# Optimization experiments

Measured on AMD Instinct MI355X. Metric: run time of the kernel, lower is better.

Reference implementation:

```python
import jax, jax.numpy as jnp
import numpy as np

N_NODES = 50000
N_EDGES = 600000
D = 128  # in_channels == out_channels
LN_EPS = 1e-5


def _mlp(h, W1, b1, W2, b2, ln_g, ln_b):
    # anemoi MLP: Linear -> SiLU -> Linear -> LayerNorm
    h = jax.nn.silu(h @ W1 + b1)
    h = h @ W2 + b2
    mu = jnp.mean(h, axis=-1, keepdims=True)
    var = jnp.var(h, axis=-1, keepdims=True)
    return (h - mu) * jax.lax.rsqrt(var + LN_EPS) * ln_g + ln_b


def setup_inputs() -> dict:
    key = jax.random.key(0)
    ks = jax.random.split(key, 12)
    s = lambda fan_in: 1.0 / np.sqrt(fan_in)
    inp = {
        "x": jax.random.normal(ks[0], (N_NODES, D), dtype=jnp.float32),
        "edge_attr": jax.random.normal(ks[1], (N_EDGES, D), dtype=jnp.float32),
        "edge_index": jax.random.randint(ks[2], (2, N_EDGES), 0, N_NODES, dtype=jnp.int32),
        # conv edge-MLP params: in = 3*D (x_dst, x_src, edge_attr)
        "eW1": jax.random.uniform(ks[3], (3 * D, D), jnp.float32, -s(3 * D), s(3 * D)),
        "eb1": jnp.zeros((D,), jnp.float32),
        "eW2": jax.random.uniform(ks[4], (D, D), jnp.float32, -s(D), s(D)),
        "eb2": jnp.zeros((D,), jnp.float32),
        "eln_g": jnp.ones((D,), jnp.float32),
        "eln_b": jnp.zeros((D,), jnp.float32),
        # node MLP params: in = 2*D (x, aggregated messages)
        "nW1": jax.random.uniform(ks[5], (2 * D, D), jnp.float32, -s(2 * D), s(2 * D)),
        "nb1": jnp.zeros((D,), jnp.float32),
        "nW2": jax.random.uniform(ks[6], (D, D), jnp.float32, -s(D), s(D)),
        "nb2": jnp.zeros((D,), jnp.float32),
        "nln_g": jnp.ones((D,), jnp.float32),
        "nln_b": jnp.zeros((D,), jnp.float32),
    }
    return inp


def reference(x, edge_attr, edge_index,
              eW1, eb1, eW2, eb2, eln_g, eln_b,
              nW1, nb1, nW2, nb2, nln_g, nln_b):
    src = edge_index[0]  # j
    dst = edge_index[1]  # i
    # GraphConv.message: edge MLP over cat([x_i, x_j, edge_attr])
    edge_in = jnp.concatenate([x[dst], x[src], edge_attr], axis=1)  # [E, 3D]
    edges_new = _mlp(edge_in, eW1, eb1, eW2, eb2, eln_g, eln_b)      # [E, D]
    # aggregate: scatter-add to destination nodes (chunking sums to the same result)
    out = jax.ops.segment_sum(edges_new, dst, num_segments=x.shape[0])  # [N, D]
    # node update: concat + MLP + residual
    nodes_new = _mlp(jnp.concatenate([x, out], axis=1), nW1, nb1, nW2, nb2, nln_g, nln_b) + x
    return nodes_new, edges_new
```

## Files before the change

kernel.cpp:

```cpp
#include <hip/hip_runtime.h>

#define D       128
#define NNODES  50000
#define NEDGES  600000
#define TE      64
#define BLK     256
#define LN_EPS  1e-5f

typedef float  fx4    __attribute__((ext_vector_type(4)));
typedef float  f32x4  __attribute__((ext_vector_type(4)));
typedef __bf16 bf16x4 __attribute__((ext_vector_type(4)));
typedef __bf16 bf16x8 __attribute__((ext_vector_type(8)));

#define EW1F_OFF 0
#define EW2F_OFF (128 * 384)
#define NW1F_OFF (EW2F_OFF + 128 * 128)
#define NW2F_OFF (NW1F_OFF + 128 * 256)
#define WS_ELEMS (NW2F_OFF + 128 * 128)

__device__ __forceinline__ float silu_f(float z) {
    return z * (1.0f / (1.0f + __expf(-z)));
}

__global__ __launch_bounds__(256) void prep_weights(
    const float* __restrict__ eW1, const float* __restrict__ eW2,
    const float* __restrict__ nW1, const float* __restrict__ nW2,
    __bf16* __restrict__ ws)
{
    int idx = blockIdx.x * 256 + threadIdx.x;
    if (idx >= WS_ELEMS) return;
    const float* src;
    int local;
    if (idx < EW2F_OFF)      { src = eW1; local = idx; }
    else if (idx < NW1F_OFF) { src = eW2; local = idx - EW2F_OFF; }
    else if (idx < NW2F_OFF) { src = nW1; local = idx - NW1F_OFF; }
    else                     { src = nW2; local = idx - NW2F_OFF; }
    const int f   = local >> 9;
    const int rem = local & 511;
    const int l   = rem >> 3;
    const int j   = rem & 7;
    const int ks  = f >> 3;
    const int nf  = f & 7;
    const int n   = (nf << 4) + (l & 15);
    const int k   = (ks << 5) + ((l >> 4) << 3) + j;
    ws[idx] = (__bf16)src[(size_t)k * D + n];
}

__global__ __launch_bounds__(BLK) void edge_kernel(
    const float* __restrict__ x,
    const float* __restrict__ edge_attr,
    const int*   __restrict__ edge_index,
    const __bf16* __restrict__ W1f,
    const float* __restrict__ b1,
    const __bf16* __restrict__ W2f,
    const float* __restrict__ b2,
    const float* __restrict__ lng, const float* __restrict__ lnb,
    float* __restrict__ edges_out,
    float* __restrict__ agg)
{
    __shared__ __bf16 in_t[TE][392];
    __shared__ int    src_s[TE], dst_s[TE];

    const int tid = threadIdx.x;
    const int e0g = blockIdx.x * TE;

    if (tid < TE) {
        src_s[tid] = edge_index[e0g + tid];
        dst_s[tid] = edge_index[NEDGES + e0g + tid];
    }
    __syncthreads();

    #pragma unroll
    for (int it = 0; it < 8; ++it) {
        const int idx = tid + it * BLK;
        const int e   = idx >> 5;
        const int c4  = (idx & 31) << 2;
        fx4 v = *(const fx4*)&x[(size_t)dst_s[e] * D + c4];
        bf16x4 h;
        #pragma unroll
        for (int j = 0; j < 4; ++j) h[j] = (__bf16)v[j];
        *(bf16x4*)&in_t[e][c4] = h;
    }
    #pragma unroll
    for (int it = 0; it < 8; ++it) {
        const int idx = tid + it * BLK;
        const int e   = idx >> 5;
        const int c4  = (idx & 31) << 2;
        fx4 v = *(const fx4*)&x[(size_t)src_s[e] * D + c4];
        bf16x4 h;
        #pragma unroll
        for (int j = 0; j < 4; ++j) h[j] = (__bf16)v[j];
        *(bf16x4*)&in_t[e][128 + c4] = h;
    }
    #pragma unroll
    for (int it = 0; it < 8; ++it) {
        const int idx = tid + it * BLK;
        const int e   = idx >> 5;
        const int c4  = (idx & 31) << 2;
        fx4 v = *(const fx4*)&edge_attr[(size_t)(e0g + e) * D + c4];
        bf16x4 h;
        #pragma unroll
        for (int j = 0; j < 4; ++j) h[j] = (__bf16)v[j];
        *(bf16x4*)&in_t[e][256 + c4] = h;
    }
    __syncthreads();

    const int lane  = tid & 63;
    const int wid   = tid >> 6;
    const int wrow0 = wid << 4;
    const int c16   = lane & 15;
    const int kq    = lane >> 4;
    const int ks8   = kq << 3;
    const int lo8   = lane << 3;

    f32x4 acc[8];
    #pragma unroll
    for (int nf = 0; nf < 8; ++nf) acc[nf] = (f32x4){0.f, 0.f, 0.f, 0.f};

    #pragma unroll
    for (int ks = 0; ks < 12; ++ks) {
        bf16x8 a = *(const bf16x8*)&in_t[wrow0 + c16][(ks << 5) + ks8];
        const __bf16* wp = W1f + ((size_t)(ks << 3) << 9) + lo8;
        #pragma unroll
        for (int nf = 0; nf < 8; ++nf) {
            bf16x8 b = *(const bf16x8*)(wp + (nf << 9));
            acc[nf] = __builtin_amdgcn_mfma_f32_16x16x32_bf16(a, b, acc[nf], 0, 0, 0);
        }
    }

    #pragma unroll
    for (int nf = 0; nf < 8; ++nf) {
        const float bb = b1[nf * 16 + c16];
        #pragma unroll
        for (int r = 0; r < 4; ++r) {
            float h = silu_f(acc[nf][r] + bb);
            in_t[wrow0 + kq * 4 + r][nf * 16 + c16] = (__bf16)h;
        }
    }

    f32x4 acc2[8];
    #pragma unroll
    for (int nf = 0; nf < 8; ++nf) acc2[nf] = (f32x4){0.f, 0.f, 0.f, 0.f};

    #pragma unroll
    for (int ks = 0; ks < 4; ++ks) {
        bf16x8 a = *(const bf16x8*)&in_t[wrow0 + c16][(ks << 5) + ks8];
        const __bf16* wp = W2f + ((size_t)(ks << 3) << 9) + lo8;
        #pragma unroll
        for (int nf = 0; nf < 8; ++nf) {
            bf16x8 b = *(const bf16x8*)(wp + (nf << 9));
            acc2[nf] = __builtin_amdgcn_mfma_f32_16x16x32_bf16(a, b, acc2[nf], 0, 0, 0);
        }
    }

    float b2v[8], gv[8], bvv[8];
    #pragma unroll
    for (int nf = 0; nf < 8; ++nf) {
        b2v[nf] = b2[nf * 16 + c16];
        gv[nf]  = lng[nf * 16 + c16];
        bvv[nf] = lnb[nf * 16 + c16];
    }

    float z[8][4];
    float s[4] = {0.f, 0.f, 0.f, 0.f}, q[4] = {0.f, 0.f, 0.f, 0.f};
    #pragma unroll
    for (int nf = 0; nf < 8; ++nf)
        #pragma unroll
        for (int r = 0; r < 4; ++r) {
            float zz = acc2[nf][r] + b2v[nf];
            z[nf][r] = zz;
            s[r] += zz;
            q[r] += zz * zz;
        }
    #pragma unroll
    for (int m = 1; m <= 8; m <<= 1)
        #pragma unroll
        for (int r = 0; r < 4; ++r) {
            s[r] += __shfl_xor(s[r], m, 64);
            q[r] += __shfl_xor(q[r], m, 64);
        }
    float mu[4], rstd[4];
    #pragma unroll
    for (int r = 0; r < 4; ++r) {
        mu[r] = s[r] * (1.0f / 128.0f);
        float var = q[r] * (1.0f / 128.0f) - mu[r] * mu[r];
        rstd[r] = rsqrtf(var + LN_EPS);
    }

    #pragma unroll
    for (int r = 0; r < 4; ++r) {
        const int row = wrow0 + kq * 4 + r;
        const size_t erow = (size_t)(e0g + row) * D;
        float* ap = agg + (size_t)dst_s[row] * D;
        #pragma unroll
        for (int nf = 0; nf < 8; ++nf) {
            const int col = nf * 16 + c16;
            float o = (z[nf][r] - mu[r]) * rstd[r] * gv[nf] + bvv[nf];
            edges_out[erow + col] = o;
            atomicAdd(ap + col, o);
        }
    }
}

__global__ __launch_bounds__(BLK) void node_kernel(
    const float* __restrict__ x,
    const float* __restrict__ agg,
    const __bf16* __restrict__ W1f,
    const float* __restrict__ b1,
    const __bf16* __restrict__ W2f,
    const float* __restrict__ b2,
    const float* __restrict__ lng, const float* __restrict__ lnb,
    float* __restrict__ nodes_out)
{
    __shared__ __bf16 in_t[TE][264];

    const int tid = threadIdx.x;
    const int r0g = blockIdx.x * TE;

    #pragma unroll
    for (int it = 0; it < 8; ++it) {
        const int idx = tid + it * BLK;
        const int e   = idx >> 5;
        const int c4  = (idx & 31) << 2;
        const int row = r0g + e;
        fx4 v = {0.f, 0.f, 0.f, 0.f};
        if (row < NNODES) v = *(const fx4*)&x[(size_t)row * D + c4];
        bf16x4 h;
        #pragma unroll
        for (int j = 0; j < 4; ++j) h[j] = (__bf16)v[j];
        *(bf16x4*)&in_t[e][c4] = h;
    }
    #pragma unroll
    for (int it = 0; it < 8; ++it) {
        const int idx = tid + it * BLK;
        const int e   = idx >> 5;
        const int c4  = (idx & 31) << 2;
        const int row = r0g + e;
        fx4 v = {0.f, 0.f, 0.f, 0.f};
        if (row < NNODES) v = *(const fx4*)&agg[(size_t)row * D + c4];
        bf16x4 h;
        #pragma unroll
        for (int j = 0; j < 4; ++j) h[j] = (__bf16)v[j];
        *(bf16x4*)&in_t[e][128 + c4] = h;
    }
    __syncthreads();

    const int lane  = tid & 63;
    const int wid   = tid >> 6;
    const int wrow0 = wid << 4;
    const int c16   = lane & 15;
    const int kq    = lane >> 4;
    const int ks8   = kq << 3;
    const int lo8   = lane << 3;

    f32x4 acc[8];
    #pragma unroll
    for (int nf = 0; nf < 8; ++nf) acc[nf] = (f32x4){0.f, 0.f, 0.f, 0.f};

    #pragma unroll
    for (int ks = 0; ks < 8; ++ks) {
        bf16x8 a = *(const bf16x8*)&in_t[wrow0 + c16][(ks << 5) + ks8];
        const __bf16* wp = W1f + ((size_t)(ks << 3) << 9) + lo8;
        #pragma unroll
        for (int nf = 0; nf < 8; ++nf) {
            bf16x8 b = *(const bf16x8*)(wp + (nf << 9));
            acc[nf] = __builtin_amdgcn_mfma_f32_16x16x32_bf16(a, b, acc[nf], 0, 0, 0);
        }
    }

    #pragma unroll
    for (int nf = 0; nf < 8; ++nf) {
        const float bb = b1[nf * 16 + c16];
        #pragma unroll
        for (int r = 0; r < 4; ++r) {
            float h = silu_f(acc[nf][r] + bb);
            in_t[wrow0 + kq * 4 + r][nf * 16 + c16] = (__bf16)h;
        }
    }

    f32x4 acc2[8];
    #pragma unroll
    for (int nf = 0; nf < 8; ++nf) acc2[nf] = (f32x4){0.f, 0.f, 0.f, 0.f};

    #pragma unroll
    for (int ks = 0; ks < 4; ++ks) {
        bf16x8 a = *(const bf16x8*)&in_t[wrow0 + c16][(ks << 5) + ks8];
        const __bf16* wp = W2f + ((size_t)(ks << 3) << 9) + lo8;
        #pragma unroll
        for (int nf = 0; nf < 8; ++nf) {
            bf16x8 b = *(const bf16x8*)(wp + (nf << 9));
            acc2[nf] = __builtin_amdgcn_mfma_f32_16x16x32_bf16(a, b, acc2[nf], 0, 0, 0);
        }
    }

    float b2v[8], gv[8], bvv[8];
    #pragma unroll
    for (int nf = 0; nf < 8; ++nf) {
        b2v[nf] = b2[nf * 16 + c16];
        gv[nf]  = lng[nf * 16 + c16];
        bvv[nf] = lnb[nf * 16 + c16];
    }

    float z[8][4];
    float s[4] = {0.f, 0.f, 0.f, 0.f}, q[4] = {0.f, 0.f, 0.f, 0.f};
    #pragma unroll
    for (int nf = 0; nf < 8; ++nf)
        #pragma unroll
        for (int r = 0; r < 4; ++r) {
            float zz = acc2[nf][r] + b2v[nf];
            z[nf][r] = zz;
            s[r] += zz;
            q[r] += zz * zz;
        }
    #pragma unroll
    for (int m = 1; m <= 8; m <<= 1)
        #pragma unroll
        for (int r = 0; r < 4; ++r) {
            s[r] += __shfl_xor(s[r], m, 64);
            q[r] += __shfl_xor(q[r], m, 64);
        }
    float mu[4], rstd[4];
    #pragma unroll
    for (int r = 0; r < 4; ++r) {
        mu[r] = s[r] * (1.0f / 128.0f);
        float var = q[r] * (1.0f / 128.0f) - mu[r] * mu[r];
        rstd[r] = rsqrtf(var + LN_EPS);
    }

    #pragma unroll
    for (int r = 0; r < 4; ++r) {
        const int row = r0g + wrow0 + kq * 4 + r;
        if (row >= NNODES) continue;
        const size_t orow = (size_t)row * D;
        #pragma unroll
        for (int nf = 0; nf < 8; ++nf) {
            const int col = nf * 16 + c16;
            float o = (z[nf][r] - mu[r]) * rstd[r] * gv[nf] + bvv[nf] + x[orow + col];
            nodes_out[orow + col] = o;
        }
    }
}

extern "C" void kernel_launch(void* const* d_in, const int* in_sizes, int n_in,
                              void* d_out, int out_size, void* d_ws, size_t ws_size,
                              hipStream_t stream) {
    (void)in_sizes; (void)n_in; (void)ws_size; (void)out_size;

    const float* x         = (const float*)d_in[0];
    const float* edge_attr = (const float*)d_in[1];
    const int*   edge_idx  = (const int*)  d_in[2];
    const float* eW1 = (const float*)d_in[3];
    const float* eb1 = (const float*)d_in[4];
    const float* eW2 = (const float*)d_in[5];
    const float* eb2 = (const float*)d_in[6];
    const float* elg = (const float*)d_in[7];
    const float* elb = (const float*)d_in[8];
    const float* nW1 = (const float*)d_in[9];
    const float* nb1 = (const float*)d_in[10];
    const float* nW2 = (const float*)d_in[11];
    const float* nb2 = (const float*)d_in[12];
    const float* nlg = (const float*)d_in[13];
    const float* nlb = (const float*)d_in[14];

    float* out       = (float*)d_out;
    float* nodes_out = out;
    float* edges_out = out + (size_t)NNODES * D;

    __bf16* ws = (__bf16*)d_ws;

    prep_weights<<<(WS_ELEMS + 255) / 256, 256, 0, stream>>>(eW1, eW2, nW1, nW2, ws);

    hipMemsetAsync(nodes_out, 0, (size_t)NNODES * D * sizeof(float), stream);

    edge_kernel<<<NEDGES / TE, BLK, 0, stream>>>(
        x, edge_attr, edge_idx,
        ws + EW1F_OFF, eb1, ws + EW2F_OFF, eb2, elg, elb,
        edges_out, nodes_out);

    node_kernel<<<(NNODES + TE - 1) / TE, BLK, 0, stream>>>(
        x, nodes_out,
        ws + NW1F_OFF, nb1, ws + NW2F_OFF, nb2, nlg, nlb,
        nodes_out);
}
```

Before: 441.3 us.

## Double edge tile per block and stream K-segments through smaller shared buffer

The edge kernel now handles 128 edges per block, with each wave computing two 16-row MFMA tiles, so every weight fragment loaded from global memory is used twice. The 384-wide input is staged one 128-column segment at a time (dst, src, edge_attr) through a 128x136 shared buffer, interleaving the gathers with the GEMM. Shared memory per block stays about the same while weight traffic per edge halves. The costs are more accumulator registers (two 8-fragment tile sets), extra barriers between segments, and less overlap of the gather with compute inside a block.

```diff
diff --git a/kernel.cpp b/kernel.cpp
--- a/kernel.cpp
+++ b/kernel.cpp
@@ -3,7 +3,8 @@
 #define D       128
 #define NNODES  50000
 #define NEDGES  600000
-#define TE      64
+#define TEE     128
+#define TN      64
 #define BLK     256
 #define LN_EPS  1e-5f
 
@@ -58,98 +59,97 @@
     float* __restrict__ edges_out,
     float* __restrict__ agg)
 {
-    __shared__ __bf16 in_t[TE][392];
-    __shared__ int    src_s[TE], dst_s[TE];
+    __shared__ __bf16 seg[TEE][136];
+    __shared__ int    src_s[TEE], dst_s[TEE];
 
     const int tid = threadIdx.x;
-    const int e0g = blockIdx.x * TE;
-
-    if (tid < TE) {
-        src_s[tid] = edge_index[e0g + tid];
-        dst_s[tid] = edge_index[NEDGES + e0g + tid];
-    }
-    __syncthreads();
-
-    #pragma unroll
-    for (int it = 0; it < 8; ++it) {
-        const int idx = tid + it * BLK;
-        const int e   = idx >> 5;
-        const int c4  = (idx & 31) << 2;
-        fx4 v = *(const fx4*)&x[(size_t)dst_s[e] * D + c4];
-        bf16x4 h;
-        #pragma unroll
-        for (int j = 0; j < 4; ++j) h[j] = (__bf16)v[j];
-        *(bf16x4*)&in_t[e][c4] = h;
-    }
-    #pragma unroll
-    for (int it = 0; it < 8; ++it) {
-        const int idx = tid + it * BLK;
-        const int e   = idx >> 5;
-        const int c4  = (idx & 31) << 2;
-        fx4 v = *(const fx4*)&x[(size_t)src_s[e] * D + c4];
-        bf16x4 h;
-        #pragma unroll
-        for (int j = 0; j < 4; ++j) h[j] = (__bf16)v[j];
-        *(bf16x4*)&in_t[e][128 + c4] = h;
-    }
-    #pragma unroll
-    for (int it = 0; it < 8; ++it) {
-        const int idx = tid + it * BLK;
-        const int e   = idx >> 5;
-        const int c4  = (idx & 31) << 2;
-        fx4 v = *(const fx4*)&edge_attr[(size_t)(e0g + e) * D + c4];
-        bf16x4 h;
-        #pragma unroll
-        for (int j = 0; j < 4; ++j) h[j] = (__bf16)v[j];
-        *(bf16x4*)&in_t[e][256 + c4] = h;
-    }
-    __syncthreads();
+    const int e0g = blockIdx.x * TEE;
+
+    if (tid < TEE) {
+        const int ge = e0g + tid;
+        src_s[tid] = (ge < NEDGES) ? edge_index[ge] : 0;
+        dst_s[tid] = (ge < NEDGES) ? edge_index[NEDGES + ge] : 0;
+    }
 
     const int lane  = tid & 63;
     const int wid   = tid >> 6;
-    const int wrow0 = wid << 4;
+    const int wrow0 = wid << 5;
     const int c16   = lane & 15;
     const int kq    = lane >> 4;
     const int ks8   = kq << 3;
     const int lo8   = lane << 3;
 
-    f32x4 acc[8];
-    #pragma unroll
-    for (int nf = 0; nf < 8; ++nf) acc[nf] = (f32x4){0.f, 0.f, 0.f, 0.f};
-
-    #pragma unroll
-    for (int ks = 0; ks < 12; ++ks) {
-        bf16x8 a = *(const bf16x8*)&in_t[wrow0 + c16][(ks << 5) + ks8];
-        const __bf16* wp = W1f + ((size_t)(ks << 3) << 9) + lo8;
+    f32x4 acc[2][8];
+    #pragma unroll
+    for (int mi = 0; mi < 2; ++mi)
+        #pragma unroll
+        for (int nf = 0; nf < 8; ++nf) acc[mi][nf] = (f32x4){0.f, 0.f, 0.f, 0.f};
+
+    #pragma unroll
+    for (int sgi = 0; sgi < 3; ++sgi) {
+        __syncthreads();
+        #pragma unroll
+        for (int it = 0; it < 16; ++it) {
+            const int idx = tid + it * BLK;
+            const int e   = idx >> 5;
+            const int c4  = (idx & 31) << 2;
+            fx4 v;
+            if (sgi == 0)      v = *(const fx4*)&x[(size_t)dst_s[e] * D + c4];
+            else if (sgi == 1) v = *(const fx4*)&x[(size_t)src_s[e] * D + c4];
+            else {
+                const int ge = e0g + e;
+                if (ge < NEDGES) v = *(const fx4*)&edge_attr[(size_t)ge * D + c4];
+                else             v = (fx4){0.f, 0.f, 0.f, 0.f};
+            }
+            bf16x4 h;
+            #pragma unroll
+            for (int j = 0; j < 4; ++j) h[j] = (__bf16)v[j];
+            *(bf16x4*)&seg[e][c4] = h;
+        }
+        __syncthreads();
+
+        #pragma unroll
+        for (int ks2 = 0; ks2 < 4; ++ks2) {
+            bf16x8 a0 = *(const bf16x8*)&seg[wrow0 + c16][(ks2 << 5) + ks8];
+            bf16x8 a1 = *(const bf16x8*)&seg[wrow0 + 16 + c16][(ks2 << 5) + ks8];
+            const __bf16* wp = W1f + ((size_t)((sgi * 4 + ks2) << 3) << 9) + lo8;
+            #pragma unroll
+            for (int nf = 0; nf < 8; ++nf) {
+                bf16x8 b = *(const bf16x8*)(wp + (nf << 9));
+                acc[0][nf] = __builtin_amdgcn_mfma_f32_16x16x32_bf16(a0, b, acc[0][nf], 0, 0, 0);
+                acc[1][nf] = __builtin_amdgcn_mfma_f32_16x16x32_bf16(a1, b, acc[1][nf], 0, 0, 0);
+            }
+        }
+    }
+
+    #pragma unroll
+    for (int nf = 0; nf < 8; ++nf) {
+        const float bb = b1[nf * 16 + c16];
+        #pragma unroll
+        for (int mi = 0; mi < 2; ++mi)
+            #pragma unroll
+            for (int r = 0; r < 4; ++r) {
+                float h = silu_f(acc[mi][nf][r] + bb);
+                seg[wrow0 + mi * 16 + kq * 4 + r][nf * 16 + c16] = (__bf16)h;
+            }
+    }
+
+    f32x4 acc2[2][8];
+    #pragma unroll
+    for (int mi = 0; mi < 2; ++mi)
+        #pragma unroll
+        for (int nf = 0; nf < 8; ++nf) acc2[mi][nf] = (f32x4){0.f, 0.f, 0.f, 0.f};
+
+    #pragma unroll
+    for (int ks = 0; ks < 4; ++ks) {
+        bf16x8 a0 = *(const bf16x8*)&seg[wrow0 + c16][(ks << 5) + ks8];
+        bf16x8 a1 = *(const bf16x8*)&seg[wrow0 + 16 + c16][(ks << 5) + ks8];
+        const __bf16* wp = W2f + ((size_t)(ks << 3) << 9) + lo8;
         #pragma unroll
         for (int nf = 0; nf < 8; ++nf) {
             bf16x8 b = *(const bf16x8*)(wp + (nf << 9));
-            acc[nf] = __builtin_amdgcn_mfma_f32_16x16x32_bf16(a, b, acc[nf], 0, 0, 0);
-        }
-    }
-
-    #pragma unroll
-    for (int nf = 0; nf < 8; ++nf) {
-        const float bb = b1[nf * 16 + c16];
-        #pragma unroll
-        for (int r = 0; r < 4; ++r) {
-            float h = silu_f(acc[nf][r] + bb);
-            in_t[wrow0 + kq * 4 + r][nf * 16 + c16] = (__bf16)h;
-        }
-    }
-
-    f32x4 acc2[8];
-    #pragma unroll
-    for (int nf = 0; nf < 8; ++nf) acc2[nf] = (f32x4){0.f, 0.f, 0.f, 0.f};
-
-    #pragma unroll
-    for (int ks = 0; ks < 4; ++ks) {
-        bf16x8 a = *(const bf16x8*)&in_t[wrow0 + c16][(ks << 5) + ks8];
-        const __bf16* wp = W2f + ((size_t)(ks << 3) << 9) + lo8;
-        #pragma unroll
-        for (int nf = 0; nf < 8; ++nf) {
-            bf16x8 b = *(const bf16x8*)(wp + (nf << 9));
-            acc2[nf] = __builtin_amdgcn_mfma_f32_16x16x32_bf16(a, b, acc2[nf], 0, 0, 0);
+            acc2[0][nf] = __builtin_amdgcn_mfma_f32_16x16x32_bf16(a0, b, acc2[0][nf], 0, 0, 0);
+            acc2[1][nf] = __builtin_amdgcn_mfma_f32_16x16x32_bf16(a1, b, acc2[1][nf], 0, 0, 0);
         }
     }
 
@@ -161,43 +161,43 @@
         bvv[nf] = lnb[nf * 16 + c16];
     }
 
-    float z[8][4];
-    float s[4] = {0.f, 0.f, 0.f, 0.f}, q[4] = {0.f, 0.f, 0.f, 0.f};
-    #pragma unroll
-    for (int nf = 0; nf < 8; ++nf)
+    #pragma unroll
+    for (int mi = 0; mi < 2; ++mi) {
+        float s[4] = {0.f, 0.f, 0.f, 0.f}, q[4] = {0.f, 0.f, 0.f, 0.f};
+        #pragma unroll
+        for (int nf = 0; nf < 8; ++nf)
+            #pragma unroll
+            for (int r = 0; r < 4; ++r) {
+                float zz = acc2[mi][nf][r] + b2v[nf];
+                acc2[mi][nf][r] = zz;
+                s[r] += zz;
+                q[r] += zz * zz;
+            }
+        #pragma unroll
+        for (int m = 1; m <= 8; m <<= 1)
+            #pragma unroll
+            for (int r = 0; r < 4; ++r) {
+                s[r] += __shfl_xor(s[r], m, 64);
+                q[r] += __shfl_xor(q[r], m, 64);
+            }
         #pragma unroll
         for (int r = 0; r < 4; ++r) {
-            float zz = acc2[nf][r] + b2v[nf];
-            z[nf][r] = zz;
-            s[r] += zz;
-            q[r] += zz * zz;
-        }
-    #pragma unroll
-    for (int m = 1; m <= 8; m <<= 1)
-        #pragma unroll
-        for (int r = 0; r < 4; ++r) {
-            s[r] += __shfl_xor(s[r], m, 64);
-            q[r] += __shfl_xor(q[r], m, 64);
-        }
-    float mu[4], rstd[4];
-    #pragma unroll
-    for (int r = 0; r < 4; ++r) {
-        mu[r] = s[r] * (1.0f / 128.0f);
-        float var = q[r] * (1.0f / 128.0f) - mu[r] * mu[r];
-        rstd[r] = rsqrtf(var + LN_EPS);
-    }
-
-    #pragma unroll
-    for (int r = 0; r < 4; ++r) {
-        const int row = wrow0 + kq * 4 + r;
-        const size_t erow = (size_t)(e0g + row) * D;
-        float* ap = agg + (size_t)dst_s[row] * D;
-        #pragma unroll
-        for (int nf = 0; nf < 8; ++nf) {
-            const int col = nf * 16 + c16;
-            float o = (z[nf][r] - mu[r]) * rstd[r] * gv[nf] + bvv[nf];
-            edges_out[erow + col] = o;
-            atomicAdd(ap + col, o);
+            const float mu   = s[r] * (1.0f / 128.0f);
+            const float var  = q[r] * (1.0f / 128.0f) - mu * mu;
+            const float rstd = rsqrtf(var + LN_EPS);
+            const int row = wrow0 + mi * 16 + kq * 4 + r;
+            const int ge  = e0g + row;
+            if (ge < NEDGES) {
+                const size_t erow = (size_t)ge * D;
+                float* ap = agg + (size_t)dst_s[row] * D;
+                #pragma unroll
+                for (int nf = 0; nf < 8; ++nf) {
+                    const int col = nf * 16 + c16;
+                    float o = (acc2[mi][nf][r] - mu) * rstd * gv[nf] + bvv[nf];
+                    edges_out[erow + col] = o;
+                    atomicAdd(ap + col, o);
+                }
+            }
         }
     }
 }
@@ -212,10 +212,10 @@
     const float* __restrict__ lng, const float* __restrict__ lnb,
     float* __restrict__ nodes_out)
 {
-    __shared__ __bf16 in_t[TE][264];
+    __shared__ __bf16 in_t[TN][264];
 
     const int tid = threadIdx.x;
-    const int r0g = blockIdx.x * TE;
+    const int r0g = blockIdx.x * TN;
 
     #pragma unroll
     for (int it = 0; it < 8; ++it) {
@@ -301,14 +301,13 @@
         bvv[nf] = lnb[nf * 16 + c16];
     }
 
-    float z[8][4];
     float s[4] = {0.f, 0.f, 0.f, 0.f}, q[4] = {0.f, 0.f, 0.f, 0.f};
     #pragma unroll
     for (int nf = 0; nf < 8; ++nf)
         #pragma unroll
         for (int r = 0; r < 4; ++r) {
             float zz = acc2[nf][r] + b2v[nf];
-            z[nf][r] = zz;
+            acc2[nf][r] = zz;
             s[r] += zz;
             q[r] += zz * zz;
         }
@@ -319,23 +318,19 @@
             s[r] += __shfl_xor(s[r], m, 64);
             q[r] += __shfl_xor(q[r], m, 64);
         }
-    float mu[4], rstd[4];
+
     #pragma unroll
     for (int r = 0; r < 4; ++r) {
-        mu[r] = s[r] * (1.0f / 128.0f);
-        float var = q[r] * (1.0f / 128.0f) - mu[r] * mu[r];
-        rstd[r] = rsqrtf(var + LN_EPS);
-    }
-
-    #pragma unroll
-    for (int r = 0; r < 4; ++r) {
+        const float mu   = s[r] * (1.0f / 128.0f);
+        const float var  = q[r] * (1.0f / 128.0f) - mu * mu;
+        const float rstd = rsqrtf(var + LN_EPS);
         const int row = r0g + wrow0 + kq * 4 + r;
         if (row >= NNODES) continue;
         const size_t orow = (size_t)row * D;
         #pragma unroll
         for (int nf = 0; nf < 8; ++nf) {
             const int col = nf * 16 + c16;
-            float o = (z[nf][r] - mu[r]) * rstd[r] * gv[nf] + bvv[nf] + x[orow + col];
+            float o = (acc2[nf][r] - mu) * rstd * gv[nf] + bvv[nf] + x[orow + col];
             nodes_out[orow + col] = o;
         }
     }
@@ -372,12 +367,12 @@
 
     hipMemsetAsync(nodes_out, 0, (size_t)NNODES * D * sizeof(float), stream);
 
-    edge_kernel<<<NEDGES / TE, BLK, 0, stream>>>(
+    edge_kernel<<<(NEDGES + TEE - 1) / TEE, BLK, 0, stream>>>(
         x, edge_attr, edge_idx,
         ws + EW1F_OFF, eb1, ws + EW2F_OFF, eb2, elg, elb,
         edges_out, nodes_out);
 
-    node_kernel<<<(NNODES + TE - 1) / TE, BLK, 0, stream>>>(
+    node_kernel<<<(NNODES + TN - 1) / TN, BLK, 0, stream>>>(
         x, nodes_out,
         ws + NW1F_OFF, nb1, ws + NW2F_OFF, nb2, nlg, nlb,
         nodes_out);
```

Result: slower. 631.2 us (+43.0%).
